# Kernel tuning notes

Measured on AMD Instinct MI355X. Metric: run time of the kernel, lower is better.

## Reference

```python
import jax, jax.numpy as jnp
import numpy as np

B, S, H, N, NREL = 16, 2048, 1024, 128, 8


def setup_inputs() -> dict:
    key = jax.random.key(0)
    ks = jax.random.split(key, 8)
    word_emb = jax.random.normal(ks[0], (B, S, H), dtype=jnp.float32)
    num_ids = jax.random.randint(ks[1], (B, N), 0, S)  # all valid (no -1 padding)
    is_response = jax.random.randint(ks[2], (B, N), 0, 2).astype(jnp.int32)
    numbers = jax.random.normal(ks[3], (B, N), dtype=jnp.float32)
    scale = 1.0 / np.sqrt(H).astype(np.float32)
    w_alpha = jax.random.normal(ks[4], (H, 1), dtype=jnp.float32) * scale
    b_alpha = jnp.zeros((1,), dtype=jnp.float32)
    w_f = jax.random.normal(ks[5], (H, H), dtype=jnp.float32) * scale
    b_f = jnp.zeros((H,), dtype=jnp.float32)
    W_r = jax.random.normal(ks[6], (NREL, H, H), dtype=jnp.float32) * scale  # 8 bias-free relation linears
    return dict(word_emb=word_emb, num_ids=num_ids, is_response=is_response,
                numbers=numbers, w_alpha=w_alpha, b_alpha=b_alpha,
                w_f=w_f, b_f=b_f, W_r=W_r)


def reference(word_emb, num_ids, is_response, numbers, w_alpha, b_alpha, w_f, b_f, W_r):
    Bn, Sn, Hn = word_emb.shape
    Nn = num_ids.shape[1]
    mask = (num_ids >= 0)  # [B,N] valid-node mask (original uses -1 padding)
    idx = jnp.clip(num_ids, 0, Sn - 1)
    # per-batch gather: Init[b,n] = word_emb[b, num_ids[b,n]]  -> [B,N,H]
    Init = jnp.take_along_axis(word_emb, idx[:, :, None], axis=1)
    alpha = jax.nn.sigmoid(Init @ w_alpha + b_alpha)  # [B,N,1]
    # all 8 relation transforms of every sender node j: T[b,r,j,:] = Init[b,j] @ W_r[r].T
    T = jnp.einsum('bnh,rkh->brnk', Init, W_r)  # [B,8,N,H]
    # relation id r(b,i,j) = 4*(num_i>num_j) + 2*resp_i + resp_j
    gt = (numbers[:, :, None] > numbers[:, None, :]).astype(jnp.int32)  # [B,N,N]
    resp = (is_response == 1).astype(jnp.int32)
    R = 4 * gt + 2 * resp[:, :, None] + resp[:, None, :]  # [B,N,N]
    sel = jax.nn.one_hot(R, NREL, dtype=word_emb.dtype)  # [B,N,N,8]
    not_diag = ~jnp.eye(Nn, dtype=bool)
    # edge weight over sender j: alpha_j, valid i & j, i != j
    wgt = (alpha[:, None, :, 0] * mask[:, None, :] * mask[:, :, None]
           * not_diag[None]).astype(word_emb.dtype)  # [B,N,N]
    Temp = jnp.einsum('bijr,brjh->bih', sel * wgt[..., None], T)  # [B,N,H]
    n_nodes = mask.sum(axis=1)  # [B]
    denom = jnp.maximum(n_nodes - 1, 1).astype(word_emb.dtype)
    Temp = Temp / denom[:, None, None]
    out = jax.nn.relu(Init @ w_f + b_f + Temp)  # [B,N,H]
    return out
```

## Files before the change

kernel.cpp:

```cpp
#include <hip/hip_runtime.h>
#include <hip/hip_bf16.h>
#include <stdint.h>

#define B_ 16
#define S_ 2048
#define H_ 1024
#define N_ 128
#define M_ (B_*N_)
#define K5 5120
#define MP 2176

typedef __attribute__((ext_vector_type(8))) short s8vec;
typedef __attribute__((ext_vector_type(4))) short s4vec;
typedef __attribute__((ext_vector_type(4))) float f4vec;
typedef __hip_bfloat16 bf16;

__global__ void k_sort(const int* __restrict__ num_ids, const int* __restrict__ is_resp,
                       const float* __restrict__ numbers,
                       int* __restrict__ sigma, int* __restrict__ newgrp,
                       int* __restrict__ respv, float* __restrict__ denom) {
    int b = blockIdx.x, i = threadIdx.x;
    __shared__ float nums[N_];
    __shared__ int sig[N_];
    __shared__ int cnt;
    float ni = numbers[b*N_ + i];
    int idv = num_ids[b*N_ + i];
    int valid = (idv >= 0) ? 1 : 0;
    nums[i] = ni;
    if (i == 0) cnt = 0;
    __syncthreads();
    int p = 0;
    for (int j = 0; j < N_; ++j) {
        float nj = nums[j];
        p += (nj < ni || (nj == ni && j < i)) ? 1 : 0;
    }
    sig[p] = i;
    atomicAdd(&cnt, valid);
    __syncthreads();
    sigma[b*N_ + i] = sig[i];
    int cur = sig[i];
    int prv = (i > 0) ? sig[i-1] : 0;
    newgrp[b*N_ + i] = (i == 0 || nums[cur] != nums[prv]) ? 1 : 0;
    respv[b*N_ + i] = ((is_resp[b*N_ + i] == 1) ? 1 : 0) | (valid << 1);
    if (i == 0) denom[b] = fmaxf((float)(cnt - 1), 1.0f);
}

__global__ void k_meta(const int* __restrict__ respv, int* __restrict__ aperm,
                       int* __restrict__ iperm, int* __restrict__ meta) {
    __shared__ int s0[1024], s1[1024];
    int t = threadIdx.x;
    aperm[t] = -1; aperm[t + 1024] = -1;
    if (t < MP - 2048) aperm[t + 2048] = -1;
    int r0 = 2*t, r1 = 2*t + 1;
    int c_a = respv[r0] & 1, c_b = respv[r1] & 1;
    int a0 = 1 - c_a, b0 = 1 - c_b;
    s0[t] = a0 + b0;
    s1[t] = c_a + c_b;
    __syncthreads();
    for (int off = 1; off < 1024; off <<= 1) {
        int v0 = (t >= off) ? s0[t-off] : 0;
        int v1 = (t >= off) ? s1[t-off] : 0;
        __syncthreads();
        s0[t] += v0; s1[t] += v1;
        __syncthreads();
    }
    int C0 = s0[1023], C1 = s1[1023];
    int P0 = ((C0 + 127) >> 7) << 7;
    int ex0 = s0[t] - (a0 + b0);
    int ex1 = s1[t] - (c_a + c_b);
    int p_a = (c_a == 0) ? ex0 : P0 + ex1;
    int p_b = (c_b == 0) ? ex0 + a0 : P0 + ex1 + c_a;
    aperm[p_a] = r0; iperm[r0] = p_a;
    aperm[p_b] = r1; iperm[r1] = p_b;
    if (t == 0) { meta[0] = P0; meta[1] = C0; meta[2] = C1; }
}

__global__ void k_prep(const float* __restrict__ word_emb, const int* __restrict__ num_ids,
                       const float* __restrict__ w_alpha, const float* __restrict__ b_alpha,
                       const float* __restrict__ denom, const int* __restrict__ iperm,
                       const float* __restrict__ W_r, const float* __restrict__ w_f,
                       bf16* __restrict__ A, float* __restrict__ ascaled,
                       bf16* __restrict__ Wt) {
    __shared__ float lds[64][65];
    int bid = blockIdx.x;
    int t = threadIdx.x;
    if (bid < 2048) {
        int b = bid >> 7, n = bid & 127;
        int idv = num_ids[b*N_ + n];
        int valid = (idv >= 0) ? 1 : 0;
        int idx = idv < 0 ? 0 : (idv > S_-1 ? S_-1 : idv);
        int pr = iperm[b*N_ + n];
        const float4* row = (const float4*)(word_emb + ((size_t)b*S_ + idx)*H_);
        float4 v = row[t];
        float4 w = ((const float4*)w_alpha)[t];
        float part = v.x*w.x + v.y*w.y + v.z*w.z + v.w*w.w;
        union { s4vec v4; bf16 h[4]; } pk;
        pk.h[0] = __float2bfloat16(v.x);
        pk.h[1] = __float2bfloat16(v.y);
        pk.h[2] = __float2bfloat16(v.z);
        pk.h[3] = __float2bfloat16(v.w);
        *(s4vec*)(A + (size_t)pr*K5 + 4*H_ + t*4) = pk.v4;
#pragma unroll
        for (int off = 32; off > 0; off >>= 1) part += __shfl_down(part, off, 64);
        if ((t & 63) == 0) lds[0][t >> 6] = part;
        __syncthreads();
        if (t == 0) {
            float dot = lds[0][0] + lds[0][1] + lds[0][2] + lds[0][3] + b_alpha[0];
            float al = 1.0f / (1.0f + __expf(-dot));
            ascaled[b*N_ + n] = valid ? (al / denom[b]) : 0.0f;
        }
        return;
    }
    if (bid < 6144) {
        size_t o = ((size_t)(bid - 2048)*256 + t)*8;
        int cs = (int)(o >> 20);
        int c = cs >> 2, s = cs & 3;
        int r = ((s >> 1) << 2) + 2*c + (s & 1);
        size_t off = o & (size_t)(H_*H_ - 1);
        const float4* src = (const float4*)(W_r + (size_t)r*H_*H_ + off);
        float4 v0 = src[0], v1 = src[1];
        union { s8vec v8; bf16 h[8]; } pk;
        pk.h[0] = __float2bfloat16(v0.x); pk.h[1] = __float2bfloat16(v0.y);
        pk.h[2] = __float2bfloat16(v0.z); pk.h[3] = __float2bfloat16(v0.w);
        pk.h[4] = __float2bfloat16(v1.x); pk.h[5] = __float2bfloat16(v1.y);
        pk.h[6] = __float2bfloat16(v1.z); pk.h[7] = __float2bfloat16(v1.w);
        *(s8vec*)(Wt + (size_t)(c*5 + s)*H_*H_ + off) = pk.v8;
        return;
    }
    int bb = bid - 6144;
    int bi = bb & 15, bj = bb >> 4;
    int ty = t >> 4, tx = t & 15;
#pragma unroll
    for (int i = 0; i < 4; ++i) {
        int r = ty*4 + i;
        float4 v = *(const float4*)(w_f + (size_t)(bi*64 + r)*H_ + bj*64 + tx*4);
        lds[r][tx*4+0] = v.x; lds[r][tx*4+1] = v.y;
        lds[r][tx*4+2] = v.z; lds[r][tx*4+3] = v.w;
    }
    __syncthreads();
    bf16* d0 = Wt + (size_t)4*H_*H_;
    bf16* d1 = Wt + (size_t)9*H_*H_;
#pragma unroll
    for (int i = 0; i < 4; ++i) {
        int n = ty*4 + i;
        size_t doff = (size_t)(bj*64 + n)*H_ + bi*64 + tx*4;
        union { s4vec v4; bf16 h[4]; } pk;
#pragma unroll
        for (int j = 0; j < 4; ++j) pk.h[j] = __float2bfloat16(lds[tx*4+j][n]);
        *(s4vec*)(d0 + doff) = pk.v4;
        *(s4vec*)(d1 + doff) = pk.v4;
    }
}

__global__ void k_build(const float* __restrict__ ascaled, const int* __restrict__ sigma,
                        const int* __restrict__ newgrp, const int* __restrict__ respv,
                        const int* __restrict__ iperm, bf16* __restrict__ A) {
    int b = blockIdx.y;
    int h = blockIdx.x*64 + threadIdx.x;
    __shared__ float as_s[N_];
    __shared__ int sig_s[N_], ng_s[N_], rv_s[N_], pm_s[N_];
    for (int j = threadIdx.x; j < N_; j += 64) {
        as_s[j] = ascaled[b*N_ + j];
        sig_s[j] = sigma[b*N_ + j];
        ng_s[j] = newgrp[b*N_ + j];
        rv_s[j] = respv[b*N_ + j];
        pm_s[j] = iperm[b*N_ + j];
    }
    __syncthreads();
    const bf16* initcol = A + 4*H_ + h;
    float tot0 = 0.f, tot1 = 0.f;
#pragma unroll 8
    for (int i2 = 0; i2 < N_; ++i2) {
        float v = as_s[i2] * __bfloat162float(initcol[(size_t)pm_s[i2]*K5]);
        if (rv_s[i2] & 1) tot1 += v; else tot0 += v;
    }
    float cS0=0.f, cS1=0.f, cG0=0.f, cG1=0.f;
#pragma unroll 8
    for (int p = 0; p < N_; ++p) {
        int i2 = sig_s[p];
        if (ng_s[p]) { cS0 += cG0; cS1 += cG1; cG0 = 0.f; cG1 = 0.f; }
        float v = as_s[i2] * __bfloat162float(initcol[(size_t)pm_s[i2]*K5]);
        int resp = rv_s[i2] & 1;
        float vf = (rv_s[i2] >> 1) ? 1.0f : 0.0f;
        float G0 = cS0, G1 = cS1;
        float L0 = tot0 - G0 - (resp ? 0.f : v);
        float L1 = tot1 - G1 - (resp ? v : 0.f);
        bf16* Ar = A + (size_t)pm_s[i2]*K5 + h;
        Ar[0*H_] = __float2bfloat16(L0*vf);
        Ar[1*H_] = __float2bfloat16(L1*vf);
        Ar[2*H_] = __float2bfloat16(G0*vf);
        Ar[3*H_] = __float2bfloat16(G1*vf);
        if (resp) cG1 += v; else cG0 += v;
    }
}

#define BM 64
#define BN 64
#define BK 64
#define NSTEP (K5/BK)

__global__ __launch_bounds__(256, 4) void k_gemm(const bf16* __restrict__ A,
                                                 const bf16* __restrict__ Wt,
                                                 const int* __restrict__ meta,
                                                 const int* __restrict__ aperm,
                                                 const float* __restrict__ b_f,
                                                 float* __restrict__ out) {
    __shared__ __align__(16) bf16 As0[BM*BK], As1[BM*BK];
    __shared__ __align__(16) bf16 Bs0[BN*BK], Bs1[BN*BK];
    int tid = threadIdx.x;
    int w = tid >> 6, lane = tid & 63;
    int q = lane >> 4, r = lane & 15;
    int bid = blockIdx.x;
    int wg = (bid & 7)*68 + (bid >> 3);
    int mt = wg % 34, nt = wg / 34;
    int rowBase = mt * BM, colBase = nt * BN;
    int wm = w >> 1, wn = w & 1;
    int P0 = meta[0];
    const bf16* Wtc = Wt + ((rowBase >= P0) ? (size_t)5*H_*H_ : 0);

    int og[2][4];
    float bias[2];
#pragma unroll
    for (int mi = 0; mi < 2; ++mi) {
        int rb = rowBase + wm*32 + mi*16 + q*4;
#pragma unroll
        for (int e = 0; e < 4; ++e) og[mi][e] = aperm[rb + e];
    }
#pragma unroll
    for (int ni = 0; ni < 2; ++ni) bias[ni] = b_f[colBase + wn*32 + ni*16 + r];
#pragma unroll
    for (int mi = 0; mi < 2; ++mi)
#pragma unroll
        for (int e = 0; e < 4; ++e) asm volatile("" : "+v"(og[mi][e]));
    asm volatile("" : "+v"(bias[0]), "+v"(bias[1]));

    f4vec acc[2][2];
#pragma unroll
    for (int mi = 0; mi < 2; ++mi)
#pragma unroll
        for (int ni = 0; ni < 2; ++ni)
#pragma unroll
            for (int e = 0; e < 4; ++e) acc[mi][ni][e] = 0.0f;

    auto STAGE = [&](bf16* AsB, bf16* BsB, int kin) {
        int slot = kin >> 10, koff = kin & 1023;
        const bf16* Wslot = Wtc + ((size_t)slot << 20);
#pragma unroll
        for (int j = 0; j < 2; ++j) {
            int c = tid + j*256;
            int row = c >> 3;
            int p = (c & 7) ^ (row & 7);
            const bf16* ga = A + (size_t)(rowBase + row)*K5 + kin + p*8;
            __builtin_amdgcn_global_load_lds((const __attribute__((address_space(1))) void*)ga,
                (__attribute__((address_space(3))) void*)((char*)AsB + j*4096 + w*1024), 16, 0, 0);
            const bf16* gb = Wslot + ((size_t)(colBase + row) << 10) + koff + p*8;
            __builtin_amdgcn_global_load_lds((const __attribute__((address_space(1))) void*)gb,
                (__attribute__((address_space(3))) void*)((char*)BsB + j*4096 + w*1024), 16, 0, 0);
        }
    };

    auto COMPUTE = [&](const bf16* AsB, const bf16* BsB) {
        const short* Asp = (const short*)AsB;
        const short* Bsp = (const short*)BsB;
        s8vec af[2][2], bfr[2][2];
#pragma unroll
        for (int kk = 0; kk < 2; ++kk) {
            int sl = ((kk*4 + q) ^ (r & 7)) << 3;
#pragma unroll
            for (int mi = 0; mi < 2; ++mi)
                af[kk][mi] = *(const s8vec*)(Asp + (wm*32 + mi*16 + r)*BK + sl);
#pragma unroll
            for (int ni = 0; ni < 2; ++ni)
                bfr[kk][ni] = *(const s8vec*)(Bsp + (wn*32 + ni*16 + r)*BK + sl);
        }
#pragma unroll
        for (int kk = 0; kk < 2; ++kk)
#pragma unroll
            for (int mi = 0; mi < 2; ++mi)
#pragma unroll
                for (int ni = 0; ni < 2; ++ni)
                    acc[mi][ni] = __builtin_amdgcn_mfma_f32_16x16x32_bf16(
                        af[kk][mi], bfr[kk][ni], acc[mi][ni], 0, 0, 0);
    };

    STAGE(As0, Bs0, 0);
    asm volatile("s_waitcnt vmcnt(0)" ::: "memory");
    __builtin_amdgcn_s_barrier();
    __builtin_amdgcn_sched_barrier(0);

    bf16 *cA = As0, *cB = Bs0, *nA = As1, *nB = Bs1;
    for (int t = 0; t < NSTEP; ++t) {
        if (t + 1 < NSTEP) STAGE(nA, nB, (t + 1)*BK);
        COMPUTE(cA, cB);
        asm volatile("s_waitcnt vmcnt(0)" ::: "memory");
        __builtin_amdgcn_s_barrier();
        __builtin_amdgcn_sched_barrier(0);
        bf16* tA = cA; cA = nA; nA = tA;
        bf16* tB = cB; cB = nB; nB = tB;
    }

#pragma unroll
    for (int mi = 0; mi < 2; ++mi) {
#pragma unroll
        for (int ni = 0; ni < 2; ++ni) {
            int cc = colBase + wn*32 + ni*16 + r;
            if (og[mi][0] >= 0) out[(size_t)og[mi][0]*H_ + cc] = fmaxf(acc[mi][ni][0] + bias[ni], 0.0f);
            if (og[mi][1] >= 0) out[(size_t)og[mi][1]*H_ + cc] = fmaxf(acc[mi][ni][1] + bias[ni], 0.0f);
            if (og[mi][2] >= 0) out[(size_t)og[mi][2]*H_ + cc] = fmaxf(acc[mi][ni][2] + bias[ni], 0.0f);
            if (og[mi][3] >= 0) out[(size_t)og[mi][3]*H_ + cc] = fmaxf(acc[mi][ni][3] + bias[ni], 0.0f);
        }
    }
}

extern "C" void kernel_launch(void* const* d_in, const int* in_sizes, int n_in,
                              void* d_out, int out_size, void* d_ws, size_t ws_size,
                              hipStream_t stream) {
    (void)in_sizes; (void)n_in; (void)out_size; (void)ws_size;
    const float* word_emb = (const float*)d_in[0];
    const int*   num_ids  = (const int*)d_in[1];
    const int*   is_resp  = (const int*)d_in[2];
    const float* numbers  = (const float*)d_in[3];
    const float* w_alpha  = (const float*)d_in[4];
    const float* b_alpha  = (const float*)d_in[5];
    const float* w_f      = (const float*)d_in[6];
    const float* b_f      = (const float*)d_in[7];
    const float* W_r      = (const float*)d_in[8];
    float* out = (float*)d_out;

    char* ws = (char*)d_ws;
    bf16*  Aws     = (bf16*)(ws);
    bf16*  Wt      = (bf16*)(ws + 22282240);
    float* ascaled = (float*)(ws + 52166656);
    int*   sigma   = (int*)(ws + 52174848);
    int*   newgrp  = (int*)(ws + 52183040);
    int*   respv   = (int*)(ws + 52191232);
    float* denom   = (float*)(ws + 52199424);
    int*   aperm   = (int*)(ws + 52199488);
    int*   iperm   = (int*)(ws + 52208192);
    int*   meta    = (int*)(ws + 52216384);

    k_sort  <<<16,   128, 0, stream>>>(num_ids, is_resp, numbers, sigma, newgrp, respv, denom);
    k_meta  <<<1,   1024, 0, stream>>>(respv, aperm, iperm, meta);
    k_prep  <<<6400, 256, 0, stream>>>(word_emb, num_ids, w_alpha, b_alpha, denom, iperm,
                                       W_r, w_f, Aws, ascaled, Wt);
    k_build <<<dim3(16,16), 64, 0, stream>>>(ascaled, sigma, newgrp, respv, iperm, Aws);
    k_gemm  <<<544,  256, 0, stream>>>(Aws, Wt, meta, aperm, b_f, out);
}
```

Before: 319.2 us.

## Split GEMM K dimension across two wave groups per block with LDS reduction

The GEMM block grows from 256 to 512 threads. Each group of four waves processes half of the K range in its own double-buffered LDS region, and the upper half's partial accumulators are added into the lower half through shared memory before the epilogue. This aims to give the 544-block grid more waves in flight to hide memory latency on a K-heavy GEMM. The cost is 64KB of LDS per block, which limits blocks per CU, plus an extra reduction and sync step. The two halves also share barriers, so one group can stall the other.

Result: faster. 309.4 us (-3.1%).

```diff
diff --git a/kernel.cpp b/kernel.cpp
--- a/kernel.cpp
+++ b/kernel.cpp
@@ -197,42 +197,53 @@
 #define BM 64
 #define BN 64
 #define BK 64
-#define NSTEP (K5/BK)
-
-__global__ __launch_bounds__(256, 4) void k_gemm(const bf16* __restrict__ A,
+#define KHALF 2560
+#define NSTEP (KHALF/BK)
+
+__global__ __launch_bounds__(512, 4) void k_gemm(const bf16* __restrict__ A,
                                                  const bf16* __restrict__ Wt,
                                                  const int* __restrict__ meta,
                                                  const int* __restrict__ aperm,
                                                  const float* __restrict__ b_f,
                                                  float* __restrict__ out) {
-    __shared__ __align__(16) bf16 As0[BM*BK], As1[BM*BK];
-    __shared__ __align__(16) bf16 Bs0[BN*BK], Bs1[BN*BK];
+    __shared__ __align__(16) char pool[65536];
     int tid = threadIdx.x;
     int w = tid >> 6, lane = tid & 63;
+    int half = w >> 2, wsub = w & 3;
+    int ht = tid & 255;
+    int hw = ht >> 6;
     int q = lane >> 4, r = lane & 15;
     int bid = blockIdx.x;
     int wg = (bid & 7)*68 + (bid >> 3);
     int mt = wg % 34, nt = wg / 34;
     int rowBase = mt * BM, colBase = nt * BN;
-    int wm = w >> 1, wn = w & 1;
+    int wm = wsub >> 1, wn = wsub & 1;
     int P0 = meta[0];
     const bf16* Wtc = Wt + ((rowBase >= P0) ? (size_t)5*H_*H_ : 0);
+    const int kbase = half * KHALF;
+
+    bf16* As0 = (bf16*)(pool + half*32768);
+    bf16* As1 = (bf16*)(pool + half*32768 +  8192);
+    bf16* Bs0 = (bf16*)(pool + half*32768 + 16384);
+    bf16* Bs1 = (bf16*)(pool + half*32768 + 24576);
 
     int og[2][4];
     float bias[2];
-#pragma unroll
-    for (int mi = 0; mi < 2; ++mi) {
-        int rb = rowBase + wm*32 + mi*16 + q*4;
-#pragma unroll
-        for (int e = 0; e < 4; ++e) og[mi][e] = aperm[rb + e];
-    }
-#pragma unroll
-    for (int ni = 0; ni < 2; ++ni) bias[ni] = b_f[colBase + wn*32 + ni*16 + r];
-#pragma unroll
-    for (int mi = 0; mi < 2; ++mi)
-#pragma unroll
-        for (int e = 0; e < 4; ++e) asm volatile("" : "+v"(og[mi][e]));
-    asm volatile("" : "+v"(bias[0]), "+v"(bias[1]));
+    if (half == 0) {
+#pragma unroll
+        for (int mi = 0; mi < 2; ++mi) {
+            int rb = rowBase + wm*32 + mi*16 + q*4;
+#pragma unroll
+            for (int e = 0; e < 4; ++e) og[mi][e] = aperm[rb + e];
+        }
+#pragma unroll
+        for (int ni = 0; ni < 2; ++ni) bias[ni] = b_f[colBase + wn*32 + ni*16 + r];
+#pragma unroll
+        for (int mi = 0; mi < 2; ++mi)
+#pragma unroll
+            for (int e = 0; e < 4; ++e) asm volatile("" : "+v"(og[mi][e]));
+        asm volatile("" : "+v"(bias[0]), "+v"(bias[1]));
+    }
 
     f4vec acc[2][2];
 #pragma unroll
@@ -247,15 +258,15 @@
         const bf16* Wslot = Wtc + ((size_t)slot << 20);
 #pragma unroll
         for (int j = 0; j < 2; ++j) {
-            int c = tid + j*256;
+            int c = ht + j*256;
             int row = c >> 3;
             int p = (c & 7) ^ (row & 7);
             const bf16* ga = A + (size_t)(rowBase + row)*K5 + kin + p*8;
             __builtin_amdgcn_global_load_lds((const __attribute__((address_space(1))) void*)ga,
-                (__attribute__((address_space(3))) void*)((char*)AsB + j*4096 + w*1024), 16, 0, 0);
+                (__attribute__((address_space(3))) void*)((char*)AsB + j*4096 + hw*1024), 16, 0, 0);
             const bf16* gb = Wslot + ((size_t)(colBase + row) << 10) + koff + p*8;
             __builtin_amdgcn_global_load_lds((const __attribute__((address_space(1))) void*)gb,
-                (__attribute__((address_space(3))) void*)((char*)BsB + j*4096 + w*1024), 16, 0, 0);
+                (__attribute__((address_space(3))) void*)((char*)BsB + j*4096 + hw*1024), 16, 0, 0);
         }
     };
 
@@ -283,14 +294,14 @@
                         af[kk][mi], bfr[kk][ni], acc[mi][ni], 0, 0, 0);
     };
 
-    STAGE(As0, Bs0, 0);
+    STAGE(As0, Bs0, kbase);
     asm volatile("s_waitcnt vmcnt(0)" ::: "memory");
     __builtin_amdgcn_s_barrier();
     __builtin_amdgcn_sched_barrier(0);
 
     bf16 *cA = As0, *cB = Bs0, *nA = As1, *nB = Bs1;
     for (int t = 0; t < NSTEP; ++t) {
-        if (t + 1 < NSTEP) STAGE(nA, nB, (t + 1)*BK);
+        if (t + 1 < NSTEP) STAGE(nA, nB, kbase + (t + 1)*BK);
         COMPUTE(cA, cB);
         asm volatile("s_waitcnt vmcnt(0)" ::: "memory");
         __builtin_amdgcn_s_barrier();
@@ -299,15 +310,37 @@
         bf16* tB = cB; cB = nB; nB = tB;
     }
 
-#pragma unroll
-    for (int mi = 0; mi < 2; ++mi) {
-#pragma unroll
-        for (int ni = 0; ni < 2; ++ni) {
-            int cc = colBase + wn*32 + ni*16 + r;
-            if (og[mi][0] >= 0) out[(size_t)og[mi][0]*H_ + cc] = fmaxf(acc[mi][ni][0] + bias[ni], 0.0f);
-            if (og[mi][1] >= 0) out[(size_t)og[mi][1]*H_ + cc] = fmaxf(acc[mi][ni][1] + bias[ni], 0.0f);
-            if (og[mi][2] >= 0) out[(size_t)og[mi][2]*H_ + cc] = fmaxf(acc[mi][ni][2] + bias[ni], 0.0f);
-            if (og[mi][3] >= 0) out[(size_t)og[mi][3]*H_ + cc] = fmaxf(acc[mi][ni][3] + bias[ni], 0.0f);
+    float* xch = (float*)pool;
+    if (half == 1) {
+#pragma unroll
+        for (int mi = 0; mi < 2; ++mi)
+#pragma unroll
+            for (int ni = 0; ni < 2; ++ni) {
+                int f = (wsub*2 + mi)*2 + ni;
+                *(f4vec*)(xch + ((size_t)f*64 + lane)*4) = acc[mi][ni];
+            }
+    }
+    __syncthreads();
+    if (half == 0) {
+#pragma unroll
+        for (int mi = 0; mi < 2; ++mi)
+#pragma unroll
+            for (int ni = 0; ni < 2; ++ni) {
+                int f = (wsub*2 + mi)*2 + ni;
+                f4vec o = *(const f4vec*)(xch + ((size_t)f*64 + lane)*4);
+#pragma unroll
+                for (int e = 0; e < 4; ++e) acc[mi][ni][e] += o[e];
+            }
+#pragma unroll
+        for (int mi = 0; mi < 2; ++mi) {
+#pragma unroll
+            for (int ni = 0; ni < 2; ++ni) {
+                int cc = colBase + wn*32 + ni*16 + r;
+                if (og[mi][0] >= 0) out[(size_t)og[mi][0]*H_ + cc] = fmaxf(acc[mi][ni][0] + bias[ni], 0.0f);
+                if (og[mi][1] >= 0) out[(size_t)og[mi][1]*H_ + cc] = fmaxf(acc[mi][ni][1] + bias[ni], 0.0f);
+                if (og[mi][2] >= 0) out[(size_t)og[mi][2]*H_ + cc] = fmaxf(acc[mi][ni][2] + bias[ni], 0.0f);
+                if (og[mi][3] >= 0) out[(size_t)og[mi][3]*H_ + cc] = fmaxf(acc[mi][ni][3] + bias[ni], 0.0f);
+            }
         }
     }
 }
@@ -344,5 +377,5 @@
     k_prep  <<<6400, 256, 0, stream>>>(word_emb, num_ids, w_alpha, b_alpha, denom, iperm,
                                        W_r, w_f, Aws, ascaled, Wt);
     k_build <<<dim3(16,16), 64, 0, stream>>>(ascaled, sigma, newgrp, respv, iperm, Aws);
-    k_gemm  <<<544,  256, 0, stream>>>(Aws, Wt, meta, aperm, b_f, out);
-}
+    k_gemm  <<<544,  512, 0, stream>>>(Aws, Wt, meta, aperm, b_f, out);
+}
```

## Deepen GEMM pipeline to four LDS stages and merge sort/meta kernels

Applied to the files above, without the earlier changes.

The GEMM main loop moves from double buffering with a full vmcnt(0) wait every step to a four-stage LDS ring with partial vmcnt(8) waits. This keeps up to three tiles of global loads in flight while MFMAs run, and launch bounds drop to 2 blocks per SM to make room for the larger LDS footprint. Separately, the per-batch sort kernel and the single-block prefix-scan kernel are fused into one 1024-thread launch, removing a launch and a round trip through global memory. The cost is lower occupancy in the GEMM and a serial sort done by one block.

After: 309.3 us. -3.1%, faster.

```diff
diff --git a/kernel.cpp b/kernel.cpp
--- a/kernel.cpp
+++ b/kernel.cpp
@@ -15,63 +15,71 @@
 typedef __attribute__((ext_vector_type(4))) float f4vec;
 typedef __hip_bfloat16 bf16;
 
-__global__ void k_sort(const int* __restrict__ num_ids, const int* __restrict__ is_resp,
-                       const float* __restrict__ numbers,
-                       int* __restrict__ sigma, int* __restrict__ newgrp,
-                       int* __restrict__ respv, float* __restrict__ denom) {
-    int b = blockIdx.x, i = threadIdx.x;
-    __shared__ float nums[N_];
-    __shared__ int sig[N_];
-    __shared__ int cnt;
-    float ni = numbers[b*N_ + i];
-    int idv = num_ids[b*N_ + i];
-    int valid = (idv >= 0) ? 1 : 0;
-    nums[i] = ni;
-    if (i == 0) cnt = 0;
-    __syncthreads();
-    int p = 0;
-    for (int j = 0; j < N_; ++j) {
-        float nj = nums[j];
-        p += (nj < ni || (nj == ni && j < i)) ? 1 : 0;
-    }
-    sig[p] = i;
-    atomicAdd(&cnt, valid);
-    __syncthreads();
-    sigma[b*N_ + i] = sig[i];
-    int cur = sig[i];
-    int prv = (i > 0) ? sig[i-1] : 0;
-    newgrp[b*N_ + i] = (i == 0 || nums[cur] != nums[prv]) ? 1 : 0;
-    respv[b*N_ + i] = ((is_resp[b*N_ + i] == 1) ? 1 : 0) | (valid << 1);
-    if (i == 0) denom[b] = fmaxf((float)(cnt - 1), 1.0f);
-}
-
-__global__ void k_meta(const int* __restrict__ respv, int* __restrict__ aperm,
-                       int* __restrict__ iperm, int* __restrict__ meta) {
+__global__ void k_sortmeta(const int* __restrict__ num_ids, const int* __restrict__ is_resp,
+                           const float* __restrict__ numbers,
+                           int* __restrict__ sigma, int* __restrict__ newgrp,
+                           int* __restrict__ respv, float* __restrict__ denom,
+                           int* __restrict__ aperm, int* __restrict__ iperm,
+                           int* __restrict__ meta) {
+    __shared__ float nums_s[2048];
+    __shared__ int sig_s[2048];
     __shared__ int s0[1024], s1[1024];
+    __shared__ int cnt_s[16];
     int t = threadIdx.x;
+    int g0 = 2*t, g1 = 2*t + 1;
+    int b = g0 >> 7;
+    int i0 = g0 & 127, i1 = g1 & 127;
+    float n0 = numbers[g0], n1 = numbers[g1];
+    int id0 = num_ids[g0], id1 = num_ids[g1];
+    int v0 = (id0 >= 0) ? 1 : 0, v1 = (id1 >= 0) ? 1 : 0;
+    int rsp0 = (is_resp[g0] == 1) ? 1 : 0, rsp1 = (is_resp[g1] == 1) ? 1 : 0;
+    nums_s[g0] = n0; nums_s[g1] = n1;
+    if (t < 16) cnt_s[t] = 0;
     aperm[t] = -1; aperm[t + 1024] = -1;
     if (t < MP - 2048) aperm[t + 2048] = -1;
-    int r0 = 2*t, r1 = 2*t + 1;
-    int c_a = respv[r0] & 1, c_b = respv[r1] & 1;
-    int a0 = 1 - c_a, b0 = 1 - c_b;
+    __syncthreads();
+    const float* nb = nums_s + b*N_;
+    int p0 = 0, p1 = 0;
+    for (int j = 0; j < N_; ++j) {
+        float nj = nb[j];
+        p0 += (nj < n0 || (nj == n0 && j < i0)) ? 1 : 0;
+        p1 += (nj < n1 || (nj == n1 && j < i1)) ? 1 : 0;
+    }
+    sig_s[b*N_ + p0] = i0;
+    sig_s[b*N_ + p1] = i1;
+    atomicAdd(&cnt_s[b], v0 + v1);
+    __syncthreads();
+    sigma[g0] = sig_s[g0]; sigma[g1] = sig_s[g1];
+    {
+        int cur = sig_s[g0];
+        int prv = (i0 > 0) ? sig_s[g0-1] : 0;
+        newgrp[g0] = (i0 == 0 || nb[cur] != nb[prv]) ? 1 : 0;
+        cur = sig_s[g1];
+        prv = sig_s[g1-1];
+        newgrp[g1] = (nb[cur] != nb[prv]) ? 1 : 0;
+    }
+    respv[g0] = rsp0 | (v0 << 1);
+    respv[g1] = rsp1 | (v1 << 1);
+    if (t < 16) denom[t] = fmaxf((float)(cnt_s[t] - 1), 1.0f);
+    int a0 = 1 - rsp0, b0 = 1 - rsp1;
     s0[t] = a0 + b0;
-    s1[t] = c_a + c_b;
+    s1[t] = rsp0 + rsp1;
     __syncthreads();
     for (int off = 1; off < 1024; off <<= 1) {
-        int v0 = (t >= off) ? s0[t-off] : 0;
-        int v1 = (t >= off) ? s1[t-off] : 0;
+        int w0 = (t >= off) ? s0[t-off] : 0;
+        int w1 = (t >= off) ? s1[t-off] : 0;
         __syncthreads();
-        s0[t] += v0; s1[t] += v1;
+        s0[t] += w0; s1[t] += w1;
         __syncthreads();
     }
     int C0 = s0[1023], C1 = s1[1023];
     int P0 = ((C0 + 127) >> 7) << 7;
     int ex0 = s0[t] - (a0 + b0);
-    int ex1 = s1[t] - (c_a + c_b);
-    int p_a = (c_a == 0) ? ex0 : P0 + ex1;
-    int p_b = (c_b == 0) ? ex0 + a0 : P0 + ex1 + c_a;
-    aperm[p_a] = r0; iperm[r0] = p_a;
-    aperm[p_b] = r1; iperm[r1] = p_b;
+    int ex1 = s1[t] - (rsp0 + rsp1);
+    int p_a = (rsp0 == 0) ? ex0 : P0 + ex1;
+    int p_b = (rsp1 == 0) ? ex0 + a0 : P0 + ex1 + rsp0;
+    aperm[p_a] = g0; iperm[g0] = p_a;
+    aperm[p_b] = g1; iperm[g1] = p_b;
     if (t == 0) { meta[0] = P0; meta[1] = C0; meta[2] = C1; }
 }
 
@@ -199,14 +207,14 @@
 #define BK 64
 #define NSTEP (K5/BK)
 
-__global__ __launch_bounds__(256, 4) void k_gemm(const bf16* __restrict__ A,
+__global__ __launch_bounds__(256, 2) void k_gemm(const bf16* __restrict__ A,
                                                  const bf16* __restrict__ Wt,
                                                  const int* __restrict__ meta,
                                                  const int* __restrict__ aperm,
                                                  const float* __restrict__ b_f,
                                                  float* __restrict__ out) {
-    __shared__ __align__(16) bf16 As0[BM*BK], As1[BM*BK];
-    __shared__ __align__(16) bf16 Bs0[BN*BK], Bs1[BN*BK];
+    __shared__ __align__(16) bf16 As0[BM*BK], As1[BM*BK], As2[BM*BK], As3[BM*BK];
+    __shared__ __align__(16) bf16 Bs0[BN*BK], Bs1[BN*BK], Bs2[BN*BK], Bs3[BN*BK];
     int tid = threadIdx.x;
     int w = tid >> 6, lane = tid & 63;
     int q = lane >> 4, r = lane & 15;
@@ -233,6 +241,7 @@
 #pragma unroll
         for (int e = 0; e < 4; ++e) asm volatile("" : "+v"(og[mi][e]));
     asm volatile("" : "+v"(bias[0]), "+v"(bias[1]));
+    asm volatile("s_waitcnt vmcnt(0)" ::: "memory");
 
     f4vec acc[2][2];
 #pragma unroll
@@ -283,21 +292,45 @@
                         af[kk][mi], bfr[kk][ni], acc[mi][ni], 0, 0, 0);
     };
 
+#define SLOT8(CA, CB, SA, SB, tnext)                              \
+    asm volatile("s_waitcnt vmcnt(8)" ::: "memory");              \
+    __builtin_amdgcn_s_barrier();                                 \
+    __builtin_amdgcn_sched_barrier(0);                            \
+    STAGE(SA, SB, (tnext)*BK);                                    \
+    COMPUTE(CA, CB);                                              \
+    __builtin_amdgcn_sched_barrier(0);
+
     STAGE(As0, Bs0, 0);
+    STAGE(As1, Bs1, BK);
+    STAGE(As2, Bs2, 2*BK);
+
+    for (int tt = 0; tt < NSTEP - 4; tt += 4) {
+        SLOT8(As0, Bs0, As3, Bs3, tt + 3);
+        SLOT8(As1, Bs1, As0, Bs0, tt + 4);
+        SLOT8(As2, Bs2, As1, Bs1, tt + 5);
+        SLOT8(As3, Bs3, As2, Bs2, tt + 6);
+    }
+    asm volatile("s_waitcnt vmcnt(8)" ::: "memory");
+    __builtin_amdgcn_s_barrier();
+    __builtin_amdgcn_sched_barrier(0);
+    STAGE(As3, Bs3, 79*BK);
+    COMPUTE(As0, Bs0);
+    __builtin_amdgcn_sched_barrier(0);
+    asm volatile("s_waitcnt vmcnt(8)" ::: "memory");
+    __builtin_amdgcn_s_barrier();
+    __builtin_amdgcn_sched_barrier(0);
+    COMPUTE(As1, Bs1);
+    __builtin_amdgcn_sched_barrier(0);
+    asm volatile("s_waitcnt vmcnt(4)" ::: "memory");
+    __builtin_amdgcn_s_barrier();
+    __builtin_amdgcn_sched_barrier(0);
+    COMPUTE(As2, Bs2);
+    __builtin_amdgcn_sched_barrier(0);
     asm volatile("s_waitcnt vmcnt(0)" ::: "memory");
     __builtin_amdgcn_s_barrier();
     __builtin_amdgcn_sched_barrier(0);
-
-    bf16 *cA = As0, *cB = Bs0, *nA = As1, *nB = Bs1;
-    for (int t = 0; t < NSTEP; ++t) {
-        if (t + 1 < NSTEP) STAGE(nA, nB, (t + 1)*BK);
-        COMPUTE(cA, cB);
-        asm volatile("s_waitcnt vmcnt(0)" ::: "memory");
-        __builtin_amdgcn_s_barrier();
-        __builtin_amdgcn_sched_barrier(0);
-        bf16* tA = cA; cA = nA; nA = tA;
-        bf16* tB = cB; cB = nB; nB = tB;
-    }
+    COMPUTE(As3, Bs3);
+#undef SLOT8
 
 #pragma unroll
     for (int mi = 0; mi < 2; ++mi) {
@@ -339,8 +372,8 @@
     int*   iperm   = (int*)(ws + 52208192);
     int*   meta    = (int*)(ws + 52216384);
 
-    k_sort  <<<16,   128, 0, stream>>>(num_ids, is_resp, numbers, sigma, newgrp, respv, denom);
-    k_meta  <<<1,   1024, 0, stream>>>(respv, aperm, iperm, meta);
+    k_sortmeta<<<1, 1024, 0, stream>>>(num_ids, is_resp, numbers, sigma, newgrp, respv,
+                                       denom, aperm, iperm, meta);
     k_prep  <<<6400, 256, 0, stream>>>(word_emb, num_ids, w_alpha, b_alpha, denom, iperm,
                                        W_r, w_f, Aws, ascaled, Wt);
     k_build <<<dim3(16,16), 64, 0, stream>>>(ascaled, sigma, newgrp, respv, iperm, Aws);
```
